# Kernel tuning notes

Measured on AMD Instinct MI355X. Metric: run time of the kernel, lower is better.

Reference implementation:

```python
import math
import jax, jax.numpy as jnp
import numpy as np

D_MODEL = 1024
D_HIDDEN = 2048
N_EXPERTS = 8
TOP_K = 2
CAPACITY_FACTOR = 1.25


def setup_inputs() -> dict:
    key = jax.random.key(0)
    k0, k1, k2, k3 = jax.random.split(key, 4)
    B, T = 2, 2048
    x = jax.random.normal(k0, (B, T, D_MODEL), dtype=jnp.float32)
    # torch nn.Linear stores weight as [out_features, in_features]
    w_router = jax.random.normal(k1, (N_EXPERTS, D_MODEL), dtype=jnp.float32) * 0.02
    w_gate = jax.random.normal(k2, (D_HIDDEN, D_MODEL), dtype=jnp.float32) * 0.02
    w_down = jax.random.normal(k3, (N_EXPERTS, D_MODEL, D_HIDDEN), dtype=jnp.float32) * 0.02
    return {"x": x, "w_router": w_router, "w_gate": w_gate, "w_down": w_down}


def _moe_forward(x, w_router, w_gate, w_down):
    B, T, D = x.shape
    N = B * T
    xf = x.reshape(N, D)

    # Router (computed in fp32, as in the original)
    logits = xf.astype(jnp.float32) @ w_router.T            # [N, E]
    gates = jax.nn.softmax(logits, axis=-1)                  # [N, E]
    topk_gates, topk_idx = jax.lax.top_k(gates, TOP_K)       # [N, K]

    # expert_mask[n, e] = 1 if expert e is among token n's top-k
    expert_mask = jax.nn.one_hot(topk_idx, N_EXPERTS, dtype=jnp.int32).sum(axis=1)  # [N, E]

    # Capacity masking via cumulative position within each expert's buffer
    capacity = math.ceil(N / N_EXPERTS * CAPACITY_FACTOR)
    position_in_expert = jnp.cumsum(expert_mask, axis=0) - 1
    expert_mask = expert_mask * (position_in_expert < capacity)

    keep = jnp.take_along_axis(expert_mask, topk_idx, axis=1) > 0  # [N, K]
    topk_gates = topk_gates * keep
    topk_gates = topk_gates / (topk_gates.sum(axis=-1, keepdims=True) + 1e-6)

    # Shared up-projection + SiLU (dropout = 0)
    hidden = jax.nn.silu(xf @ w_gate.T)                      # [N, H]

    # combine[n, e] = sum_k topk_gates[n, k] * [topk_idx[n, k] == e]
    combine = (topk_gates[:, :, None]
               * jax.nn.one_hot(topk_idx, N_EXPERTS, dtype=topk_gates.dtype)).sum(axis=1)  # [N, E]

    # Combine: y[n] = sum_e combine[n, e] * (hidden[n] @ w_down[e].T)
    # (dropped tokens have combine weight 0, matching the gated index_add in torch)
    y = jnp.zeros((N, D), dtype=x.dtype)
    for e in range(N_EXPERTS):  # small fixed loop over experts
        y = y + combine[:, e:e + 1] * (hidden @ w_down[e].T)
    return y.reshape(B, T, D)


def reference(x, w_router, w_gate, w_down):
    return _moe_forward(x, w_router, w_gate, w_down)
```

## Files before the change

kernel.cpp:

```cpp
#include <hip/hip_runtime.h>
#include <hip/hip_bf16.h>
#include <math.h>

#define NTOK 4096
#define DMODEL 1024
#define DHID 2048
#define NEXP 8
#define CAP 640
#define SLOTS (NEXP * CAP)
#define NWG ((size_t)DHID * DMODEL)
#define NWD ((size_t)NEXP * DMODEL * DHID)

typedef __attribute__((ext_vector_type(8))) short short8;
typedef __attribute__((ext_vector_type(4))) float f32x4;

__device__ inline short f2bf(float f) {
    union { float f; unsigned u; } v; v.f = f;
    unsigned r = v.u + 0x7FFF + ((v.u >> 16) & 1);
    return (short)(r >> 16);
}
__device__ inline float bf2f(unsigned short u) {
    union { unsigned u; float f; } v; v.u = ((unsigned)u) << 16; return v.f;
}
__device__ inline void async16(const short* g, short* l) {
    __builtin_amdgcn_global_load_lds(
        (const __attribute__((address_space(1))) unsigned*)g,
        (__attribute__((address_space(3))) unsigned*)l, 16, 0, 0);
}

__global__ __launch_bounds__(256) void prep_kernel(
        const float* __restrict__ x, const float* __restrict__ wr, short* __restrict__ Xb,
        int2* __restrict__ topk_idx, float2* __restrict__ topk_gate,
        const float* __restrict__ wg, short* __restrict__ WGb,
        const float* __restrict__ wd, short* __restrict__ WDb)
{
    {
        const size_t ci = ((size_t)blockIdx.x * 256 + threadIdx.x) * 8;
        const float* src; short* dst;
        if (ci < NWG) { src = wg + ci; dst = WGb + ci; }
        else          { src = wd + (ci - NWG); dst = WDb + (ci - NWG); }
        float4 v0 = ((const float4*)src)[0];
        float4 v1 = ((const float4*)src)[1];
        short8 s = { f2bf(v0.x), f2bf(v0.y), f2bf(v0.z), f2bf(v0.w),
                     f2bf(v1.x), f2bf(v1.y), f2bf(v1.z), f2bf(v1.w) };
        *(short8*)dst = s;
    }
    if (blockIdx.x >= NTOK / 4) return;
    const int token = blockIdx.x * 4 + (threadIdx.x >> 6);
    const int lane  = threadIdx.x & 63;
    const float* xr = x + (size_t)token * DMODEL + lane * 16;
    float4 xv[4];
#pragma unroll
    for (int j = 0; j < 4; j++) xv[j] = ((const float4*)xr)[j];
    short8 s0 = { f2bf(xv[0].x), f2bf(xv[0].y), f2bf(xv[0].z), f2bf(xv[0].w),
                  f2bf(xv[1].x), f2bf(xv[1].y), f2bf(xv[1].z), f2bf(xv[1].w) };
    short8 s1 = { f2bf(xv[2].x), f2bf(xv[2].y), f2bf(xv[2].z), f2bf(xv[2].w),
                  f2bf(xv[3].x), f2bf(xv[3].y), f2bf(xv[3].z), f2bf(xv[3].w) };
    short* xo = Xb + (size_t)token * DMODEL + lane * 16;
    *(short8*)xo = s0;
    *(short8*)(xo + 8) = s1;

    float acc[NEXP];
#pragma unroll
    for (int e = 0; e < NEXP; e++) acc[e] = 0.f;
#pragma unroll
    for (int j = 0; j < 4; j++) {
#pragma unroll
        for (int e = 0; e < NEXP; e++) {
            float4 wv = ((const float4*)(wr + e * DMODEL + lane * 16))[j];
            acc[e] += xv[j].x * wv.x + xv[j].y * wv.y + xv[j].z * wv.z + xv[j].w * wv.w;
        }
    }
#pragma unroll
    for (int off = 32; off >= 1; off >>= 1) {
#pragma unroll
        for (int e = 0; e < NEXP; e++) acc[e] += __shfl_xor(acc[e], off, 64);
    }
    if (lane == 0) {
        float m = acc[0];
#pragma unroll
        for (int e = 1; e < NEXP; e++) m = fmaxf(m, acc[e]);
        float den = 0.f, g[NEXP];
#pragma unroll
        for (int e = 0; e < NEXP; e++) { g[e] = __expf(acc[e] - m); den += g[e]; }
        float inv = 1.f / den;
#pragma unroll
        for (int e = 0; e < NEXP; e++) g[e] *= inv;
        int i0 = 0; float l0 = acc[0];
#pragma unroll
        for (int e = 1; e < NEXP; e++) if (acc[e] > l0) { l0 = acc[e]; i0 = e; }
        int i1 = -1; float l1 = -1e30f;
#pragma unroll
        for (int e = 0; e < NEXP; e++) if (e != i0 && acc[e] > l1) { l1 = acc[e]; i1 = e; }
        topk_idx[token]  = make_int2(i0, i1);
        topk_gate[token] = make_float2(g[i0], g[i1]);
    }
}

__global__ __launch_bounds__(256) void router_fb_kernel(
        const float* __restrict__ x, const float* __restrict__ wr,
        int2* __restrict__ topk_idx, float2* __restrict__ topk_gate)
{
    const int token = blockIdx.x * 4 + (threadIdx.x >> 6);
    const int lane  = threadIdx.x & 63;
    const float* xr = x + (size_t)token * DMODEL + lane * 16;
    float acc[NEXP];
#pragma unroll
    for (int e = 0; e < NEXP; e++) acc[e] = 0.f;
#pragma unroll
    for (int j = 0; j < 4; j++) {
        float4 xv = ((const float4*)xr)[j];
#pragma unroll
        for (int e = 0; e < NEXP; e++) {
            float4 wv = ((const float4*)(wr + e * DMODEL + lane * 16))[j];
            acc[e] += xv.x * wv.x + xv.y * wv.y + xv.z * wv.z + xv.w * wv.w;
        }
    }
#pragma unroll
    for (int off = 32; off >= 1; off >>= 1) {
#pragma unroll
        for (int e = 0; e < NEXP; e++) acc[e] += __shfl_xor(acc[e], off, 64);
    }
    if (lane == 0) {
        float m = acc[0];
#pragma unroll
        for (int e = 1; e < NEXP; e++) m = fmaxf(m, acc[e]);
        float den = 0.f, g[NEXP];
#pragma unroll
        for (int e = 0; e < NEXP; e++) { g[e] = __expf(acc[e] - m); den += g[e]; }
        float inv = 1.f / den;
#pragma unroll
        for (int e = 0; e < NEXP; e++) g[e] *= inv;
        int i0 = 0; float l0 = acc[0];
#pragma unroll
        for (int e = 1; e < NEXP; e++) if (acc[e] > l0) { l0 = acc[e]; i0 = e; }
        int i1 = -1; float l1 = -1e30f;
#pragma unroll
        for (int e = 0; e < NEXP; e++) if (e != i0 && acc[e] > l1) { l1 = acc[e]; i1 = e; }
        topk_idx[token]  = make_int2(i0, i1);
        topk_gate[token] = make_float2(g[i0], g[i1]);
    }
}

__global__ __launch_bounds__(1024) void scan_kernel(
        const int2* __restrict__ topk_idx, const float2* __restrict__ topk_gate,
        int* __restrict__ gtok, float* __restrict__ gw, int* __restrict__ gcnt,
        int2* __restrict__ tslot, float2* __restrict__ tw)
{
    __shared__ unsigned long long wt0[16], wt1[16];
    const int th = threadIdx.x, lane = th & 63, wid = th >> 6;
    int2 idx[4]; float2 gt[4];
#pragma unroll
    for (int j = 0; j < 4; j++) { idx[j] = topk_idx[th * 4 + j]; gt[j] = topk_gate[th * 4 + j]; }
    unsigned long long c0 = 0, c1 = 0;
#pragma unroll
    for (int j = 0; j < 4; j++) {
        int e0 = idx[j].x, e1 = idx[j].y;
        if (e0 < 4) c0 += 1ull << (e0 * 16); else c1 += 1ull << ((e0 - 4) * 16);
        if (e1 < 4) c0 += 1ull << (e1 * 16); else c1 += 1ull << ((e1 - 4) * 16);
    }
    const unsigned long long my0 = c0, my1 = c1;
#pragma unroll
    for (int d = 1; d < 64; d <<= 1) {
        unsigned long long t0 = __shfl_up(c0, d, 64);
        unsigned long long t1 = __shfl_up(c1, d, 64);
        if (lane >= d) { c0 += t0; c1 += t1; }
    }
    if (lane == 63) { wt0[wid] = c0; wt1[wid] = c1; }
    __syncthreads();
    unsigned long long o0 = 0, o1 = 0;
    for (int w = 0; w < wid; w++) { o0 += wt0[w]; o1 += wt1[w]; }
    c0 += o0; c1 += o1;
    if (th == 1023) {
#pragma unroll
        for (int e = 0; e < 4; e++) gcnt[e]     = min((int)((c0 >> (e * 16)) & 0xFFFF), CAP);
#pragma unroll
        for (int e = 0; e < 4; e++) gcnt[4 + e] = min((int)((c1 >> (e * 16)) & 0xFFFF), CAP);
    }
    const unsigned long long x0 = c0 - my0, x1 = c1 - my1;
    int base[NEXP];
#pragma unroll
    for (int e = 0; e < 4; e++) base[e]     = (int)((x0 >> (e * 16)) & 0xFFFF);
#pragma unroll
    for (int e = 0; e < 4; e++) base[4 + e] = (int)((x1 >> (e * 16)) & 0xFFFF);
#pragma unroll
    for (int j = 0; j < 4; j++) {
        const int n = th * 4 + j;
        const int e0 = idx[j].x, e1 = idx[j].y;
        const int p0 = base[e0]++;
        const int p1 = base[e1]++;
        const bool k0 = p0 < CAP, k1 = p1 < CAP;
        const float gg0 = k0 ? gt[j].x : 0.f, gg1 = k1 ? gt[j].y : 0.f;
        const float invs = 1.f / (gg0 + gg1 + 1e-6f);
        const int s0 = k0 ? e0 * CAP + p0 : 0;
        const int s1 = k1 ? e1 * CAP + p1 : 0;
        if (k0) { gtok[s0] = n; gw[s0] = gg0 * invs; }
        if (k1) { gtok[s1] = n; gw[s1] = gg1 * invs; }
        tslot[n] = make_int2(s0, s1);
        tw[n]    = make_float2(gg0 * invs, gg1 * invs);
    }
}

__global__ __launch_bounds__(256) void gemm1_kernel(
        const short* __restrict__ Xb, const short* __restrict__ WGb, short* __restrict__ Hid)
{
    __shared__ __align__(16) short As[128 * 64];
    __shared__ __align__(16) short Bs[128 * 64];
    const int t = threadIdx.x;
    const int wave = t >> 6, lane = t & 63;
    const int m0 = blockIdx.y * 128, n0 = blockIdx.x * 128;
    const int wm = (wave >> 1) * 64, wn = (wave & 1) * 64;
    const int lm = lane & 15, lq = lane >> 4;

    const short *ga[4], *gb[4];
    short *la[4], *lb[4];
#pragma unroll
    for (int j = 0; j < 4; j++) {
        const int b   = wave * 4 + j;
        const int row = (b >> 1) * 16 + lm;
        const int col = (b & 1) * 32 + lq * 8;
        la[j] = &As[b * 512 + lane * 8];
        lb[j] = &Bs[b * 512 + lane * 8];
        ga[j] = Xb  + (size_t)(m0 + row) * DMODEL + col;
        gb[j] = WGb + (size_t)(n0 + row) * DMODEL + col;
    }

    f32x4 acc[4][4];
#pragma unroll
    for (int a = 0; a < 4; a++)
#pragma unroll
        for (int b = 0; b < 4; b++) acc[a][b] = (f32x4)(0.f);

    for (int k0 = 0; k0 < DMODEL; k0 += 64) {
#pragma unroll
        for (int j = 0; j < 4; j++) { async16(ga[j] + k0, la[j]); async16(gb[j] + k0, lb[j]); }
        __syncthreads();
#pragma unroll
        for (int kk = 0; kk < 2; kk++) {
            short8 af[4], bf[4];
#pragma unroll
            for (int mi = 0; mi < 4; mi++)
                af[mi] = *(const short8*)&As[((((wm >> 4) + mi) * 2 + kk) * 64 + lane) * 8];
#pragma unroll
            for (int ni = 0; ni < 4; ni++)
                bf[ni] = *(const short8*)&Bs[((((wn >> 4) + ni) * 2 + kk) * 64 + lane) * 8];
#pragma unroll
            for (int mi = 0; mi < 4; mi++)
#pragma unroll
                for (int ni = 0; ni < 4; ni++)
                    acc[mi][ni] = __builtin_amdgcn_mfma_f32_16x16x32_bf16(af[mi], bf[ni], acc[mi][ni], 0, 0, 0);
        }
        __syncthreads();
    }
#pragma unroll
    for (int mi = 0; mi < 4; mi++)
#pragma unroll
        for (int i = 0; i < 4; i++) {
            const int row = m0 + wm + mi * 16 + lq * 4 + i;
#pragma unroll
            for (int ni = 0; ni < 4; ni++) {
                const int col = n0 + wn + ni * 16 + lm;
                const float v = acc[mi][ni][i];
                Hid[(size_t)row * DHID + col] = f2bf(v / (1.f + __expf(-v)));
            }
        }
}

__global__ __launch_bounds__(256) void gemm2_kernel(
        const short* __restrict__ Hid, const short* __restrict__ WDb,
        const int* __restrict__ gtok, const int* __restrict__ gcnt,
        short* __restrict__ Yp, int KS)
{
    __shared__ __align__(16) short As[128 * 64];
    __shared__ __align__(16) short Bs[128 * 64];
    __shared__ int tok_s[128];
    const int e  = blockIdx.x;
    const int n0 = blockIdx.y * 128;
    const int m0 = (blockIdx.z / KS) * 128;
    const int ks = blockIdx.z % KS;
    const int cnt = gcnt[e];
    if (m0 >= cnt) return;
    const int t = threadIdx.x;
    const int wave = t >> 6, lane = t & 63;
    const int wm = (wave >> 1) * 64, wn = (wave & 1) * 64;
    const int lm = lane & 15, lq = lane >> 4;
    const short* WDe = WDb + (size_t)e * DMODEL * DHID;

    if (t < 128) tok_s[t] = (m0 + t < cnt) ? gtok[e * CAP + m0 + t] : 0;
    __syncthreads();

    const short *ga[4], *gb[4];
    short *la[4], *lb[4];
#pragma unroll
    for (int j = 0; j < 4; j++) {
        const int b   = wave * 4 + j;
        const int row = (b >> 1) * 16 + lm;
        const int col = (b & 1) * 32 + lq * 8;
        la[j] = &As[b * 512 + lane * 8];
        lb[j] = &Bs[b * 512 + lane * 8];
        ga[j] = Hid + (size_t)tok_s[row] * DHID + col;
        gb[j] = WDe + (size_t)(n0 + row) * DHID + col;
    }

    f32x4 acc[4][4];
#pragma unroll
    for (int a = 0; a < 4; a++)
#pragma unroll
        for (int b = 0; b < 4; b++) acc[a][b] = (f32x4)(0.f);

    const int kbeg = ks * (DHID / KS), kend = kbeg + DHID / KS;
    for (int k0 = kbeg; k0 < kend; k0 += 64) {
#pragma unroll
        for (int j = 0; j < 4; j++) { async16(ga[j] + k0, la[j]); async16(gb[j] + k0, lb[j]); }
        __syncthreads();
#pragma unroll
        for (int kk = 0; kk < 2; kk++) {
            short8 af[4], bf[4];
#pragma unroll
            for (int mi = 0; mi < 4; mi++)
                af[mi] = *(const short8*)&As[((((wm >> 4) + mi) * 2 + kk) * 64 + lane) * 8];
#pragma unroll
            for (int ni = 0; ni < 4; ni++)
                bf[ni] = *(const short8*)&Bs[((((wn >> 4) + ni) * 2 + kk) * 64 + lane) * 8];
#pragma unroll
            for (int mi = 0; mi < 4; mi++)
#pragma unroll
                for (int ni = 0; ni < 4; ni++)
                    acc[mi][ni] = __builtin_amdgcn_mfma_f32_16x16x32_bf16(af[mi], bf[ni], acc[mi][ni], 0, 0, 0);
        }
        __syncthreads();
    }
    short* Yo = Yp + (size_t)ks * SLOTS * DMODEL;
#pragma unroll
    for (int mi = 0; mi < 4; mi++)
#pragma unroll
        for (int i = 0; i < 4; i++) {
            const int slot = e * CAP + m0 + wm + mi * 16 + lq * 4 + i;
#pragma unroll
            for (int ni = 0; ni < 4; ni++) {
                const int col = n0 + wn + ni * 16 + lm;
                Yo[(size_t)slot * DMODEL + col] = f2bf(acc[mi][ni][i]);
            }
        }
}

__global__ __launch_bounds__(256) void combine_kernel(
        const short* __restrict__ Yp, const int2* __restrict__ tslot,
        const float2* __restrict__ tw, float* __restrict__ y, int KS)
{
    const int token = blockIdx.x;
    const int c = threadIdx.x * 4;
    const int2   s = tslot[token];
    const float2 w = tw[token];
    float4 o = make_float4(0.f, 0.f, 0.f, 0.f);
    for (int ks = 0; ks < KS; ks++) {
        const unsigned short* base = (const unsigned short*)Yp + (size_t)ks * SLOTS * DMODEL;
        ushort4 a = *(const ushort4*)(base + (size_t)s.x * DMODEL + c);
        ushort4 b = *(const ushort4*)(base + (size_t)s.y * DMODEL + c);
        o.x += w.x * bf2f(a.x) + w.y * bf2f(b.x);
        o.y += w.x * bf2f(a.y) + w.y * bf2f(b.y);
        o.z += w.x * bf2f(a.z) + w.y * bf2f(b.z);
        o.w += w.x * bf2f(a.w) + w.y * bf2f(b.w);
    }
    *(float4*)&y[(size_t)token * DMODEL + c] = o;
}

__global__ __launch_bounds__(256) void gemm1_fb_kernel(
        const float* __restrict__ X, const float* __restrict__ WG, short* __restrict__ Hid)
{
    __shared__ short As[128][72];
    __shared__ short Bs[128][72];
    const int t = threadIdx.x;
    const int wave = t >> 6, lane = t & 63;
    const int m0 = blockIdx.y * 128, n0 = blockIdx.x * 128;
    const int wm = (wave >> 1) * 64, wn = (wave & 1) * 64;
    const int lm = lane & 15, lq = lane >> 4, lk = lq * 8;
    const int r0 = t >> 3, c8 = (t & 7) * 8;

    f32x4 acc[4][4];
#pragma unroll
    for (int a = 0; a < 4; a++)
#pragma unroll
        for (int b = 0; b < 4; b++) acc[a][b] = (f32x4)(0.f);

    for (int k0 = 0; k0 < DMODEL; k0 += 64) {
#pragma unroll
        for (int i = 0; i < 4; i++) {
            const int row = r0 + i * 32;
            const float* ga = X + (size_t)(m0 + row) * DMODEL + k0 + c8;
            float4 v0 = ((const float4*)ga)[0];
            float4 v1 = ((const float4*)ga)[1];
            short8 s = { f2bf(v0.x), f2bf(v0.y), f2bf(v0.z), f2bf(v0.w),
                         f2bf(v1.x), f2bf(v1.y), f2bf(v1.z), f2bf(v1.w) };
            *(short8*)&As[row][c8] = s;
            const float* gb = WG + (size_t)(n0 + row) * DMODEL + k0 + c8;
            float4 w0 = ((const float4*)gb)[0];
            float4 w1 = ((const float4*)gb)[1];
            short8 sw = { f2bf(w0.x), f2bf(w0.y), f2bf(w0.z), f2bf(w0.w),
                          f2bf(w1.x), f2bf(w1.y), f2bf(w1.z), f2bf(w1.w) };
            *(short8*)&Bs[row][c8] = sw;
        }
        __syncthreads();
#pragma unroll
        for (int kk = 0; kk < 64; kk += 32) {
            short8 af[4], bf[4];
#pragma unroll
            for (int mi = 0; mi < 4; mi++) af[mi] = *(const short8*)&As[wm + mi * 16 + lm][kk + lk];
#pragma unroll
            for (int ni = 0; ni < 4; ni++) bf[ni] = *(const short8*)&Bs[wn + ni * 16 + lm][kk + lk];
#pragma unroll
            for (int mi = 0; mi < 4; mi++)
#pragma unroll
                for (int ni = 0; ni < 4; ni++)
                    acc[mi][ni] = __builtin_amdgcn_mfma_f32_16x16x32_bf16(af[mi], bf[ni], acc[mi][ni], 0, 0, 0);
        }
        __syncthreads();
    }
#pragma unroll
    for (int mi = 0; mi < 4; mi++)
#pragma unroll
        for (int i = 0; i < 4; i++) {
            const int row = m0 + wm + mi * 16 + lq * 4 + i;
#pragma unroll
            for (int ni = 0; ni < 4; ni++) {
                const int col = n0 + wn + ni * 16 + lm;
                const float v = acc[mi][ni][i];
                const float s = v / (1.f + __expf(-v));
                Hid[(size_t)row * DHID + col] = f2bf(s);
            }
        }
}

__global__ __launch_bounds__(256) void gemm2_fb_kernel(
        const short* __restrict__ Hid, const float* __restrict__ WD,
        const int* __restrict__ gtok, const float* __restrict__ gw,
        const int* __restrict__ gcnt, float* __restrict__ Y)
{
    __shared__ short As[128][72];
    __shared__ short Bs[128][72];
    __shared__ int   tok_s[128];
    __shared__ float w_s[128];
    const int e = blockIdx.z;
    const int cnt = gcnt[e];
    const int m0 = blockIdx.y * 128;
    if (m0 >= cnt) return;
    const int n0 = blockIdx.x * 128;
    const int t = threadIdx.x;
    const int wave = t >> 6, lane = t & 63;
    const int wm = (wave >> 1) * 64, wn = (wave & 1) * 64;
    const int lm = lane & 15, lq = lane >> 4, lk = lq * 8;
    const int r0 = t >> 3, c8 = (t & 7) * 8;
    const float* WDe = WD + (size_t)e * DMODEL * DHID;

    if (t < 128) {
        const int r = m0 + t;
        const bool v = r < cnt;
        tok_s[t] = v ? gtok[e * CAP + r] : 0;
        w_s[t]   = v ? gw[e * CAP + r] : 0.f;
    }
    __syncthreads();

    f32x4 acc[4][4];
#pragma unroll
    for (int a = 0; a < 4; a++)
#pragma unroll
        for (int b = 0; b < 4; b++) acc[a][b] = (f32x4)(0.f);

    const int tokA[4] = { tok_s[r0], tok_s[r0 + 32], tok_s[r0 + 64], tok_s[r0 + 96] };

    for (int k0 = 0; k0 < DHID; k0 += 64) {
#pragma unroll
        for (int i = 0; i < 4; i++) {
            const int row = r0 + i * 32;
            uint4 av = *(const uint4*)(Hid + (size_t)tokA[i] * DHID + k0 + c8);
            *(uint4*)&As[row][c8] = av;
            const float* gb = WDe + (size_t)(n0 + row) * DHID + k0 + c8;
            float4 w0 = ((const float4*)gb)[0];
            float4 w1 = ((const float4*)gb)[1];
            short8 sw = { f2bf(w0.x), f2bf(w0.y), f2bf(w0.z), f2bf(w0.w),
                          f2bf(w1.x), f2bf(w1.y), f2bf(w1.z), f2bf(w1.w) };
            *(short8*)&Bs[row][c8] = sw;
        }
        __syncthreads();
#pragma unroll
        for (int kk = 0; kk < 64; kk += 32) {
            short8 af[4], bf[4];
#pragma unroll
            for (int mi = 0; mi < 4; mi++) af[mi] = *(const short8*)&As[wm + mi * 16 + lm][kk + lk];
#pragma unroll
            for (int ni = 0; ni < 4; ni++) bf[ni] = *(const short8*)&Bs[wn + ni * 16 + lm][kk + lk];
#pragma unroll
            for (int mi = 0; mi < 4; mi++)
#pragma unroll
                for (int ni = 0; ni < 4; ni++)
                    acc[mi][ni] = __builtin_amdgcn_mfma_f32_16x16x32_bf16(af[mi], bf[ni], acc[mi][ni], 0, 0, 0);
        }
        __syncthreads();
    }
#pragma unroll
    for (int mi = 0; mi < 4; mi++)
#pragma unroll
        for (int i = 0; i < 4; i++) {
            const int r = wm + mi * 16 + lq * 4 + i;
            const float wr = w_s[r];
            if (wr > 0.f) {
                const int token = tok_s[r];
#pragma unroll
                for (int ni = 0; ni < 4; ni++) {
                    const int col = n0 + wn + ni * 16 + lm;
                    atomicAdd(&Y[(size_t)token * DMODEL + col], acc[mi][ni][i] * wr);
                }
            }
        }
}

extern "C" void kernel_launch(void* const* d_in, const int* in_sizes, int n_in,
                              void* d_out, int out_size, void* d_ws, size_t ws_size,
                              hipStream_t stream) {
    const float* x  = (const float*)d_in[0];
    const float* wr = (const float*)d_in[1];
    const float* wg = (const float*)d_in[2];
    const float* wd = (const float*)d_in[3];
    float* y = (float*)d_out;

    char* w = (char*)d_ws;
    int2*   topk_idx  = (int2*)w;    w += NTOK * sizeof(int2);
    float2* topk_gate = (float2*)w;  w += NTOK * sizeof(float2);
    int*    gtok      = (int*)w;     w += NEXP * CAP * sizeof(int);
    float*  gw        = (float*)w;   w += NEXP * CAP * sizeof(float);
    int*    gcnt      = (int*)w;     w += 256;
    int2*   tslot     = (int2*)w;    w += NTOK * sizeof(int2);
    float2* tw        = (float2*)w;  w += NTOK * sizeof(float2);
    short*  Hid       = (short*)w;   w += (size_t)NTOK * DHID * sizeof(short);
    short*  WDb       = (short*)w;   w += (size_t)NEXP * DMODEL * DHID * sizeof(short);
    short*  Xb        = (short*)w;
    short*  WGb       = (short*)(w + (size_t)NTOK * DMODEL * sizeof(short));
    short*  Yp        = (short*)w;
    const size_t span12 = ((size_t)NTOK * DMODEL + (size_t)DHID * DMODEL) * sizeof(short);
    const size_t need63 = (size_t)(w - (char*)d_ws) + span12;
    const size_t need96 = (size_t)(w - (char*)d_ws) + (size_t)4 * SLOTS * DMODEL * 2;

    if (ws_size >= need63) {
        const int KS2 = (ws_size >= need96) ? 4 : 1;
        prep_kernel<<<(int)((NWG + NWD) / 2048), 256, 0, stream>>>(
            x, wr, Xb, topk_idx, topk_gate, wg, WGb, wd, WDb);
        scan_kernel<<<1, 1024, 0, stream>>>(topk_idx, topk_gate, gtok, gw, gcnt, tslot, tw);
        gemm1_kernel<<<dim3(DHID / 128, NTOK / 128), 256, 0, stream>>>(Xb, WGb, Hid);
        gemm2_kernel<<<dim3(NEXP, DMODEL / 128, (CAP / 128) * KS2), 256, 0, stream>>>(
            Hid, WDb, gtok, gcnt, Yp, KS2);
        combine_kernel<<<NTOK, 256, 0, stream>>>(Yp, tslot, tw, y, KS2);
    } else {
        hipMemsetAsync(y, 0, (size_t)NTOK * DMODEL * sizeof(float), stream);
        router_fb_kernel<<<NTOK / 4, 256, 0, stream>>>(x, wr, topk_idx, topk_gate);
        scan_kernel<<<1, 1024, 0, stream>>>(topk_idx, topk_gate, gtok, gw, gcnt, tslot, tw);
        gemm1_fb_kernel<<<dim3(DHID / 128, NTOK / 128), 256, 0, stream>>>(x, wg, Hid);
        gemm2_fb_kernel<<<dim3(DMODEL / 128, (CAP + 127) / 128, NEXP), 256, 0, stream>>>(
            Hid, wd, gtok, gw, gcnt, y);
    }
}
```

Before: 238.5 us.

## Move down-proj weight bf16 conversion into gemm1 launch to overlap with GEMM

The fp32-to-bf16 conversion of the expert down-projection weights moves out of the prep kernel into extra blocks appended to the gemm1 grid. Those blocks run alongside the up-projection GEMM tiles, so the memory-bound conversion can overlap with compute. The prep kernel now handles only the router, the activation conversion and the gate weight conversion, with separate block ranges instead of every block doing conversion work. The risk is that the conversion blocks compete with GEMM tiles for bandwidth and CU slots.

```diff
diff --git a/kernel.cpp b/kernel.cpp
--- a/kernel.cpp
+++ b/kernel.cpp
@@ -31,21 +31,17 @@
 __global__ __launch_bounds__(256) void prep_kernel(
         const float* __restrict__ x, const float* __restrict__ wr, short* __restrict__ Xb,
         int2* __restrict__ topk_idx, float2* __restrict__ topk_gate,
-        const float* __restrict__ wg, short* __restrict__ WGb,
-        const float* __restrict__ wd, short* __restrict__ WDb)
-{
-    {
-        const size_t ci = ((size_t)blockIdx.x * 256 + threadIdx.x) * 8;
-        const float* src; short* dst;
-        if (ci < NWG) { src = wg + ci; dst = WGb + ci; }
-        else          { src = wd + (ci - NWG); dst = WDb + (ci - NWG); }
-        float4 v0 = ((const float4*)src)[0];
-        float4 v1 = ((const float4*)src)[1];
+        const float* __restrict__ wg, short* __restrict__ WGb)
+{
+    if (blockIdx.x >= NTOK / 4) {
+        const size_t ci = ((size_t)(blockIdx.x - NTOK / 4) * 256 + threadIdx.x) * 8;
+        float4 v0 = ((const float4*)(wg + ci))[0];
+        float4 v1 = ((const float4*)(wg + ci))[1];
         short8 s = { f2bf(v0.x), f2bf(v0.y), f2bf(v0.z), f2bf(v0.w),
                      f2bf(v1.x), f2bf(v1.y), f2bf(v1.z), f2bf(v1.w) };
-        *(short8*)dst = s;
-    }
-    if (blockIdx.x >= NTOK / 4) return;
+        *(short8*)(WGb + ci) = s;
+        return;
+    }
     const int token = blockIdx.x * 4 + (threadIdx.x >> 6);
     const int lane  = threadIdx.x & 63;
     const float* xr = x + (size_t)token * DMODEL + lane * 16;
@@ -202,8 +198,19 @@
 }
 
 __global__ __launch_bounds__(256) void gemm1_kernel(
-        const short* __restrict__ Xb, const short* __restrict__ WGb, short* __restrict__ Hid)
-{
+        const short* __restrict__ Xb, const short* __restrict__ WGb, short* __restrict__ Hid,
+        const float* __restrict__ wd, short* __restrict__ WDb)
+{
+    if (blockIdx.y >= NTOK / 128) {
+        const size_t cb = (size_t)(blockIdx.y - NTOK / 128) * 16 + blockIdx.x;
+        const size_t ci = (cb * 256 + threadIdx.x) * 8;
+        float4 v0 = ((const float4*)(wd + ci))[0];
+        float4 v1 = ((const float4*)(wd + ci))[1];
+        short8 s = { f2bf(v0.x), f2bf(v0.y), f2bf(v0.z), f2bf(v0.w),
+                     f2bf(v1.x), f2bf(v1.y), f2bf(v1.z), f2bf(v1.w) };
+        *(short8*)(WDb + ci) = s;
+        return;
+    }
     __shared__ __align__(16) short As[128 * 64];
     __shared__ __align__(16) short Bs[128 * 64];
     const int t = threadIdx.x;
@@ -542,10 +549,11 @@
 
     if (ws_size >= need63) {
         const int KS2 = (ws_size >= need96) ? 4 : 1;
-        prep_kernel<<<(int)((NWG + NWD) / 2048), 256, 0, stream>>>(
-            x, wr, Xb, topk_idx, topk_gate, wg, WGb, wd, WDb);
+        prep_kernel<<<NTOK / 4 + (int)(NWG / 2048), 256, 0, stream>>>(
+            x, wr, Xb, topk_idx, topk_gate, wg, WGb);
         scan_kernel<<<1, 1024, 0, stream>>>(topk_idx, topk_gate, gtok, gw, gcnt, tslot, tw);
-        gemm1_kernel<<<dim3(DHID / 128, NTOK / 128), 256, 0, stream>>>(Xb, WGb, Hid);
+        gemm1_kernel<<<dim3(DHID / 128, NTOK / 128 + (int)(NWD / 2048 / (DHID / 128))), 256, 0, stream>>>(
+            Xb, WGb, Hid, wd, WDb);
         gemm2_kernel<<<dim3(NEXP, DMODEL / 128, (CAP / 128) * KS2), 256, 0, stream>>>(
             Hid, WDb, gtok, gcnt, Yp, KS2);
         combine_kernel<<<NTOK, 256, 0, stream>>>(Yp, tslot, tw, y, KS2);
```

Result: no change. 239.4 us (+0.4%).
